# Optimization experiments

Hardware: AMD Instinct MI355X
Metric: run time of the kernel (lower is better)

## Reference

```python
import jax, jax.numpy as jnp
import numpy as np

N_NODES = 100000
N_EDGES = 1600000
N_GRAPHS = 1024
B = 1024
GNN_INP, GNN_HID, GNN_OUT = 64, 128, 64
INP, HID, OUT = 64, 256, 1
EPS = 1e-5  # torch BatchNorm1d default eps


def _bn(h, gamma, beta):
    # training-mode BatchNorm1d: biased batch statistics over dim 0
    m = h.mean(axis=0)
    v = jnp.mean((h - m) ** 2, axis=0)
    return (h - m) * jax.lax.rsqrt(v + EPS) * gamma + beta


def setup_inputs() -> dict:
    key = jax.random.key(0)
    ks = jax.random.split(key, 24)
    s = 0.05
    inp = {
        "x": jax.random.normal(ks[0], (B, INP), jnp.float32),
        "masks": jax.random.randint(ks[1], (B,), 0, N_GRAPHS),
        "gnn_x": jax.random.normal(ks[2], (N_NODES, GNN_INP), jnp.float32),
        "edge_index": jax.random.randint(ks[3], (2, N_EDGES), 0, N_NODES),
        "gnn_batch": jnp.sort(jax.random.randint(ks[4], (N_NODES,), 0, N_GRAPHS)),
        # GCNConv params
        "W_gcn": jax.random.normal(ks[5], (GNN_INP, GNN_HID), jnp.float32) * s,
        "b_gcn": jnp.zeros((GNN_HID,), jnp.float32),
        "g1": jnp.ones((GNN_HID,), jnp.float32), "be1": jnp.zeros((GNN_HID,), jnp.float32),
        "W_lin1": jax.random.normal(ks[6], (GNN_HID, GNN_HID // 2), jnp.float32) * s,
        "b_lin1": jnp.zeros((GNN_HID // 2,), jnp.float32),
        "g2": jnp.ones((GNN_HID // 2,), jnp.float32), "be2": jnp.zeros((GNN_HID // 2,), jnp.float32),
        "W_lin2": jax.random.normal(ks[7], (GNN_HID // 2, GNN_OUT), jnp.float32) * s,
        "b_lin2": jnp.zeros((GNN_OUT,), jnp.float32),
        "g3": jnp.ones((GNN_OUT,), jnp.float32), "be3": jnp.zeros((GNN_OUT,), jnp.float32),
        # head params
        "W_fc1": jax.random.normal(ks[8], (INP + GNN_OUT, HID), jnp.float32) * s,
        "b_fc1": jnp.zeros((HID,), jnp.float32),
        "g4": jnp.ones((HID,), jnp.float32), "be4": jnp.zeros((HID,), jnp.float32),
        "W_fc2": jax.random.normal(ks[9], (HID, HID // 4), jnp.float32) * s,
        "b_fc2": jnp.zeros((HID // 4,), jnp.float32),
        "g5": jnp.ones((HID // 4,), jnp.float32), "be5": jnp.zeros((HID // 4,), jnp.float32),
        "W_fc3": jax.random.normal(ks[10], (HID // 4, OUT), jnp.float32) * s,
        "b_fc3": jnp.zeros((OUT,), jnp.float32),
    }
    return inp


def _forward(x, masks, gnn_x, edge_index, gnn_batch,
             W_gcn, b_gcn, g1, be1, W_lin1, b_lin1, g2, be2, W_lin2, b_lin2,
             g3, be3, W_fc1, b_fc1, g4, be4, W_fc2, b_fc2, g5, be5, W_fc3, b_fc3):
    N = gnn_x.shape[0]
    # --- GCNConv: linear transform, self-loops, sym-normalized scatter-add ---
    h = gnn_x @ W_gcn  # [N, GNN_HID]
    loop = jnp.arange(N)
    src = jnp.concatenate([edge_index[0], loop])
    dst = jnp.concatenate([edge_index[1], loop])
    deg = jax.ops.segment_sum(jnp.ones_like(dst, jnp.float32), dst, num_segments=N)
    dis = jax.lax.rsqrt(deg)  # deg >= 1 thanks to self-loops
    norm = dis[src] * dis[dst]  # [E+N]
    agg = jax.ops.segment_sum(h[src] * norm[:, None], dst, num_segments=N) + b_gcn
    z = jax.nn.relu(_bn(agg, g1, be1))  # dropout = identity (eval)
    # --- global_mean_pool over graph ids ---
    sums = jax.ops.segment_sum(z, gnn_batch, num_segments=N_GRAPHS)
    cnt = jax.ops.segment_sum(jnp.ones((N,), jnp.float32), gnn_batch, num_segments=N_GRAPHS)
    pooled = sums / jnp.maximum(cnt, 1.0)[:, None]  # [G, GNN_HID]
    z = jax.nn.relu(_bn(pooled @ W_lin1 + b_lin1, g2, be2))
    z = _bn(z @ W_lin2 + b_lin2, g3, be3)  # [G, GNN_OUT]
    # --- MixGNN head ---
    g = z[masks]  # [B, GNN_OUT]
    t = jnp.concatenate([x, g], axis=1)
    t = jax.nn.relu(_bn(t @ W_fc1 + b_fc1, g4, be4))
    t = t * t  # Multiply([h, h])
    t = jax.nn.relu(_bn(t @ W_fc2 + b_fc2, g5, be5))
    t = t * t
    t = t * t
    return t @ W_fc3 + b_fc3  # [B, OUT]


def reference(x, masks, gnn_x, edge_index, gnn_batch,
              W_gcn, b_gcn, g1, be1, W_lin1, b_lin1, g2, be2, W_lin2, b_lin2,
              g3, be3, W_fc1, b_fc1, g4, be4, W_fc2, b_fc2, g5, be5, W_fc3, b_fc3):
    return _forward(x, masks, gnn_x, edge_index, gnn_batch,
                    W_gcn, b_gcn, g1, be1, W_lin1, b_lin1, g2, be2, W_lin2, b_lin2,
                    g3, be3, W_fc1, b_fc1, g4, be4, W_fc2, b_fc2, g5, be5, W_fc3, b_fc3)
```

## Files before the change

### kernel.cpp

```cpp
#include <hip/hip_runtime.h>
#include <hip/hip_bf16.h>

#define N_NODES 100000
#define N_EDGES 1600000
#define N_GRAPHS 1024
#define BSZ 1024
#define EPS 1e-5f

#define NBUCK 256
#define BUCKW 391
#define SRC_MASK 0x1FFFF
#define BIN_CHUNK 16384
#define BIN_BLOCKS 98
#define STAGE_CAP 16384

#define WS_GHIST   0
#define WS_BNAGG   256
#define WS_STATS1  512
#define WS_STATS2  640
#define WS_STATS4  768
#define WS_STATS5  1280
#define WS_ZTOTAL  1408
#define WS_GBASE   1408
#define WS_GCUR    1664
#define WS_GSTART  1920
#define WS_DIS     2948
#define WS_ROWPTR  102948
#define WS_PACKED  202952
#define WS_CSRC    1802952
#define WS_SCALE1  3402952
#define WS_SHIFT1  3403080
#define WS_AGGX    3403208
#define WS_AGG     9803208
#define WS_POOLED  22603208
#define WS_T1      22734280
#define WS_T2      22799816
#define WS_T4      22865352
#define WS_T5      23127496

__global__ void zero_kernel(float* __restrict__ p, int n) {
    int i = blockIdx.x * blockDim.x + threadIdx.x;
    int stride = gridDim.x * blockDim.x;
    for (; i < n; i += stride) p[i] = 0.0f;
}

__global__ __launch_bounds__(256) void hist_kernel(const int* __restrict__ dst,
                                                   int* __restrict__ ghist) {
    __shared__ int lh[NBUCK];
    int tid = threadIdx.x;
    lh[tid] = 0;
    __syncthreads();
    for (int i = blockIdx.x * 256 + tid; i < N_EDGES; i += gridDim.x * 256)
        atomicAdd(&lh[dst[i] / BUCKW], 1);
    __syncthreads();
    if (lh[tid]) atomicAdd(&ghist[tid], lh[tid]);
}

__global__ __launch_bounds__(256) void scan_kernel(const int* __restrict__ ghist,
                                                   int* __restrict__ gbase,
                                                   int* __restrict__ gcursor) {
    __shared__ int ls[NBUCK];
    int tid = threadIdx.x;
    int v = ghist[tid];
    ls[tid] = v;
    for (int off = 1; off < NBUCK; off <<= 1) {
        __syncthreads();
        int t = (tid >= off) ? ls[tid - off] : 0;
        __syncthreads();
        ls[tid] += t;
    }
    __syncthreads();
    int excl = ls[tid] - v;
    gbase[tid] = excl;
    gcursor[tid] = excl;
}

__global__ __launch_bounds__(1024) void bin_kernel(const int* __restrict__ ei,
                                                   int* __restrict__ gcursor,
                                                   unsigned int* __restrict__ packed) {
    __shared__ unsigned int stage[BIN_CHUNK];
    __shared__ int lh[NBUCK], lbase[NBUCK], lcur[NBUCK], gb[NBUCK];
    const int* src = ei;
    const int* dst = ei + N_EDGES;
    int tid = threadIdx.x;
    int base = blockIdx.x * BIN_CHUNK;
    int n = min(BIN_CHUNK, N_EDGES - base);
    if (tid < NBUCK) lh[tid] = 0;
    __syncthreads();
    for (int i = tid; i < n; i += 1024)
        atomicAdd(&lh[dst[base + i] / BUCKW], 1);
    __syncthreads();
    if (tid < NBUCK) lbase[tid] = lh[tid];
    __syncthreads();
    for (int off = 1; off < NBUCK; off <<= 1) {
        int t = (tid < NBUCK && tid >= off) ? lbase[tid - off] : 0;
        __syncthreads();
        if (tid < NBUCK) lbase[tid] += t;
        __syncthreads();
    }
    if (tid < NBUCK) {
        int excl = lbase[tid] - lh[tid];
        lbase[tid] = excl;
        lcur[tid] = excl;
        gb[tid] = atomicAdd(&gcursor[tid], lh[tid]);
    }
    __syncthreads();
    for (int i = tid; i < n; i += 1024) {
        int d = dst[base + i];
        int s = src[base + i];
        int bk = d / BUCKW;
        int dl = d - bk * BUCKW;
        int slot = atomicAdd(&lcur[bk], 1);
        stage[slot] = ((unsigned int)dl << 17) | (unsigned int)s;
    }
    __syncthreads();
    int wid = tid >> 6, lane = tid & 63;
    for (int bk = wid; bk < NBUCK; bk += 16) {
        int lo = lbase[bk], len = lh[bk], go = gb[bk];
        for (int j = lane; j < len; j += 64)
            packed[go + j] = stage[lo + j];
    }
}

__global__ __launch_bounds__(256) void csr_build_kernel(const unsigned int* __restrict__ packed,
                                                        const int* __restrict__ gbase,
                                                        const int* __restrict__ ghist,
                                                        int* __restrict__ rowptr,
                                                        int* __restrict__ csrc,
                                                        float* __restrict__ dis) {
    __shared__ int dcnt[BUCKW];
    __shared__ int lcur[BUCKW];
    __shared__ int stage[STAGE_CAP];
    int b = blockIdx.x, tid = threadIdx.x;
    int e0 = gbase[b], ecnt = ghist[b];
    int nbase = b * BUCKW;
    int nmax = min(BUCKW, N_NODES - nbase);
    for (int i = tid; i < BUCKW; i += 256) dcnt[i] = 0;
    __syncthreads();
    for (int i = tid; i < ecnt; i += 256)
        atomicAdd(&dcnt[packed[e0 + i] >> 17], 1);
    __syncthreads();
    for (int i = tid; i < nmax; i += 256)
        dis[nbase + i] = rsqrtf((float)dcnt[i] + 1.0f);
    __syncthreads();
    if (tid < 64) {
        int lane = tid;
        int run = 0;
        for (int c = 0; c < BUCKW; c += 64) {
            int idx = c + lane;
            int v = (idx < BUCKW) ? dcnt[idx] : 0;
            int inc = v;
#pragma unroll
            for (int off = 1; off < 64; off <<= 1) {
                int t = __shfl_up(inc, off);
                if (lane >= off) inc += t;
            }
            if (idx < BUCKW) {
                int excl = run + inc - v;
                dcnt[idx] = excl;
                lcur[idx] = excl;
            }
            run += __shfl(inc, 63);
        }
    }
    __syncthreads();
    for (int i = tid; i < nmax; i += 256)
        rowptr[nbase + i] = e0 + dcnt[i];
    if (b == 0 && tid == 0) rowptr[N_NODES] = N_EDGES;
    if (ecnt <= STAGE_CAP) {
        for (int i = tid; i < ecnt; i += 256) {
            unsigned int r = packed[e0 + i];
            int slot = atomicAdd(&lcur[r >> 17], 1);
            stage[slot] = (int)(r & SRC_MASK);
        }
        __syncthreads();
        for (int i = tid; i < ecnt; i += 256) csrc[e0 + i] = stage[i];
    } else {
        for (int i = tid; i < ecnt; i += 256) {
            unsigned int r = packed[e0 + i];
            int slot = atomicAdd(&lcur[r >> 17], 1);
            csrc[e0 + slot] = (int)(r & SRC_MASK);
        }
    }
}

__global__ __launch_bounds__(256) void gather_kernel(const float* __restrict__ x,
                                                     const int* __restrict__ rowptr,
                                                     const int* __restrict__ csrc,
                                                     const float* __restrict__ dis,
                                                     float* __restrict__ aggx) {
    int wid = (blockIdx.x * 256 + threadIdx.x) >> 6;
    int lane = threadIdx.x & 63;
    if (wid >= N_NODES) return;
    int start = rowptr[wid];
    int end = rowptr[wid + 1];
    float dd = dis[wid];
    float acc = x[(size_t)wid * 64 + lane] * dd * dd;
    for (int j0 = start; j0 < end; j0 += 64) {
        int cnt = min(64, end - j0);
        int sv = 0;
        float wv = 0.f;
        if (lane < cnt) {
            sv = csrc[j0 + lane];
            wv = dis[sv] * dd;
        }
        int iters = (cnt + 7) & ~7;
        for (int k = 0; k < iters; k += 8) {
            int s[8]; float w[8], v[8];
#pragma unroll
            for (int u = 0; u < 8; ++u) {
                s[u] = __shfl(sv, k + u);
                w[u] = __shfl(wv, k + u);
            }
#pragma unroll
            for (int u = 0; u < 8; ++u) v[u] = x[(size_t)s[u] * 64 + lane];
#pragma unroll
            for (int u = 0; u < 8; ++u) acc = fmaf(v[u], w[u], acc);
        }
    }
    aggx[(size_t)wid * 64 + lane] = acc;
}

__global__ __launch_bounds__(256) void gemm_agg_kernel(const float* __restrict__ A,
                                                       const float* __restrict__ W,
                                                       const float* __restrict__ bias,
                                                       float* __restrict__ AGG) {
    __shared__ float Ws[64 * 128];
    __shared__ float As[16 * 64];
    int tid = threadIdx.x;
    const float4* W4 = (const float4*)W;
    float4* Ws4 = (float4*)Ws;
#pragma unroll
    for (int i = 0; i < 8; ++i) Ws4[tid + i * 256] = W4[tid + i * 256];
    int row0 = blockIdx.x * 16;
    ((float4*)As)[tid] = ((const float4*)(A + (size_t)row0 * 64))[tid];
    __syncthreads();
    int tx = tid & 31;
    int ty = tid >> 5;
    int r0 = ty * 2;
    float4 bb = ((const float4*)bias)[tx];
    float acc[2][4] = {{bb.x, bb.y, bb.z, bb.w}, {bb.x, bb.y, bb.z, bb.w}};
#pragma unroll
    for (int k = 0; k < 64; ++k) {
        float a0 = As[r0 * 64 + k];
        float a1 = As[(r0 + 1) * 64 + k];
        float4 w = Ws4[k * 32 + tx];
        acc[0][0] += a0 * w.x; acc[0][1] += a0 * w.y; acc[0][2] += a0 * w.z; acc[0][3] += a0 * w.w;
        acc[1][0] += a1 * w.x; acc[1][1] += a1 * w.y; acc[1][2] += a1 * w.z; acc[1][3] += a1 * w.w;
    }
#pragma unroll
    for (int rr = 0; rr < 2; ++rr) {
        float4 v = make_float4(acc[rr][0], acc[rr][1], acc[rr][2], acc[rr][3]);
        ((float4*)(AGG + (size_t)(row0 + r0 + rr) * 128))[tx] = v;
    }
}

__global__ __launch_bounds__(256) void bnagg_stats_kernel(const float* __restrict__ agg,
                                                          float* __restrict__ stats) {
    __shared__ float4 ls[256];
    int tid = threadIdx.x;
    int lane = tid & 63;
    int grp = tid >> 6;
    int f = lane * 2;
    float2 s = {0.f, 0.f}, sq = {0.f, 0.f};
    for (int r = blockIdx.x * 4 + grp; r < N_NODES; r += gridDim.x * 4) {
        float2 a = *(const float2*)(agg + (size_t)r * 128 + f);
        s.x += a.x; s.y += a.y;
        sq.x += a.x * a.x; sq.y += a.y * a.y;
    }
    ls[tid] = make_float4(s.x, s.y, sq.x, sq.y);
    __syncthreads();
    if (tid < 64) {
        float4 v = ls[tid];
        float4 b = ls[tid + 64], c = ls[tid + 128], d = ls[tid + 192];
        v.x += b.x + c.x + d.x;
        v.y += b.y + c.y + d.y;
        v.z += b.z + c.z + d.z;
        v.w += b.w + c.w + d.w;
        unsafeAtomicAdd(&stats[f], v.x);
        unsafeAtomicAdd(&stats[f + 1], v.y);
        unsafeAtomicAdd(&stats[128 + f], v.z);
        unsafeAtomicAdd(&stats[128 + f + 1], v.w);
    }
}

__global__ void bn1_fold_kernel(const float* __restrict__ stats, const float* __restrict__ g1,
                                const float* __restrict__ be1, float* __restrict__ scale1,
                                float* __restrict__ shift1) {
    int f = threadIdx.x;
    float m = stats[f] * (1.0f / N_NODES);
    float var = stats[128 + f] * (1.0f / N_NODES) - m * m;
    float sc = g1[f] * rsqrtf(var + EPS);
    scale1[f] = sc;
    shift1[f] = be1[f] - m * sc;
}

__global__ __launch_bounds__(1024) void graph_bounds_kernel(const int* __restrict__ batch,
                                                            int* __restrict__ gstart) {
    int g = threadIdx.x;
    int lo = 0, hi = N_NODES;
    while (lo < hi) {
        int mid = (lo + hi) >> 1;
        if (batch[mid] < g) lo = mid + 1; else hi = mid;
    }
    gstart[g] = lo;
    if (g == 0) gstart[N_GRAPHS] = N_NODES;
}

__global__ __launch_bounds__(256) void pool_gather_kernel(const float* __restrict__ agg,
                                                          const int* __restrict__ gstart,
                                                          const float* __restrict__ scale1,
                                                          const float* __restrict__ shift1,
                                                          float* __restrict__ pooled) {
    int g = (blockIdx.x * 256 + threadIdx.x) >> 6;
    int lane = threadIdx.x & 63;
    if (g >= N_GRAPHS) return;
    int r0 = gstart[g], r1 = gstart[g + 1];
    int f = lane * 2;
    float2 sc = *(const float2*)(scale1 + f);
    float2 sh = *(const float2*)(shift1 + f);
    float2 acc = {0.f, 0.f};
    for (int r = r0; r < r1; ++r) {
        float2 a = *(const float2*)(agg + (size_t)r * 128 + f);
        acc.x += fmaxf(a.x * sc.x + sh.x, 0.f);
        acc.y += fmaxf(a.y * sc.y + sh.y, 0.f);
    }
    float inv = 1.0f / fmaxf((float)(r1 - r0), 1.0f);
    float2 o; o.x = acc.x * inv; o.y = acc.y * inv;
    *(float2*)(pooled + (size_t)g * 128 + f) = o;
}

__global__ __launch_bounds__(256) void lin1_kernel(const float* __restrict__ pooled,
                                                   const float* __restrict__ W,
                                                   const float* __restrict__ bias,
                                                   float* __restrict__ t1,
                                                   float* __restrict__ stats1) {
    __shared__ float ls[256], ls2[256];
    int tid = threadIdx.x;
    int r = blockIdx.x * 4 + (tid >> 6);
    int c = tid & 63;
    float acc = bias[c];
    const float* srow = pooled + (size_t)r * 128;
#pragma unroll 8
    for (int k = 0; k < 128; ++k)
        acc += srow[k] * W[k * 64 + c];
    t1[r * 64 + c] = acc;
    ls[tid] = acc; ls2[tid] = acc * acc;
    __syncthreads();
    if (tid < 64) {
        float s = ls[tid] + ls[tid + 64] + ls[tid + 128] + ls[tid + 192];
        float q = ls2[tid] + ls2[tid + 64] + ls2[tid + 128] + ls2[tid + 192];
        unsafeAtomicAdd(&stats1[c], s);
        unsafeAtomicAdd(&stats1[64 + c], q);
    }
}

__global__ __launch_bounds__(256) void lin2_kernel(const float* __restrict__ t1,
                                                   const float* __restrict__ stats1,
                                                   const float* __restrict__ g,
                                                   const float* __restrict__ be,
                                                   const float* __restrict__ W,
                                                   const float* __restrict__ bias,
                                                   float* __restrict__ t2,
                                                   float* __restrict__ stats2) {
    __shared__ float sc[64], sh[64];
    __shared__ float ls[256], ls2[256];
    int tid = threadIdx.x;
    if (tid < 64) {
        float m = stats1[tid] * (1.0f / BSZ);
        float var = stats1[64 + tid] * (1.0f / BSZ) - m * m;
        float s = g[tid] * rsqrtf(var + EPS);
        sc[tid] = s; sh[tid] = be[tid] - m * s;
    }
    __syncthreads();
    int r = blockIdx.x * 4 + (tid >> 6);
    int c = tid & 63;
    float acc = bias[c];
    const float* row = t1 + (size_t)r * 64;
#pragma unroll 8
    for (int k = 0; k < 64; ++k) {
        float z = fmaxf(row[k] * sc[k] + sh[k], 0.f);
        acc += z * W[k * 64 + c];
    }
    t2[r * 64 + c] = acc;
    ls[tid] = acc; ls2[tid] = acc * acc;
    __syncthreads();
    if (tid < 64) {
        float s = ls[tid] + ls[tid + 64] + ls[tid + 128] + ls[tid + 192];
        float q = ls2[tid] + ls2[tid + 64] + ls2[tid + 128] + ls2[tid + 192];
        unsafeAtomicAdd(&stats2[c], s);
        unsafeAtomicAdd(&stats2[64 + c], q);
    }
}

__global__ __launch_bounds__(1024) void fc1_kernel(const float* __restrict__ x,
                                                   const int* __restrict__ masks,
                                                   const float* __restrict__ t2,
                                                   const float* __restrict__ stats2,
                                                   const float* __restrict__ g3,
                                                   const float* __restrict__ be3,
                                                   const float* __restrict__ W,
                                                   const float* __restrict__ bias,
                                                   float* __restrict__ t4,
                                                   float* __restrict__ stats4) {
    __shared__ float sc[64], sh[64];
    __shared__ float cat[4][128];
    __shared__ float ls[1024], ls2[1024];
    int tid = threadIdx.x;
    if (tid < 64) {
        float m = stats2[tid] * (1.0f / BSZ);
        float var = stats2[64 + tid] * (1.0f / BSZ) - m * m;
        float s = g3[tid] * rsqrtf(var + EPS);
        sc[tid] = s; sh[tid] = be3[tid] - m * s;
    }
    __syncthreads();
    int r0 = blockIdx.x * 4;
    if (tid < 512) {
        int i = tid >> 7;
        int k = tid & 127;
        int r = r0 + i;
        float v;
        if (k < 64) {
            v = x[r * 64 + k];
        } else {
            int mrow = masks[r];
            int kk = k - 64;
            v = t2[mrow * 64 + kk] * sc[kk] + sh[kk];
        }
        cat[i][k] = v;
    }
    __syncthreads();
    int i = tid >> 8;
    int c = tid & 255;
    float acc = bias[c];
#pragma unroll 8
    for (int k = 0; k < 128; ++k)
        acc += cat[i][k] * W[k * 256 + c];
    t4[(size_t)(r0 + i) * 256 + c] = acc;
    ls[tid] = acc; ls2[tid] = acc * acc;
    __syncthreads();
    if (tid < 256) {
        float s = ls[tid] + ls[tid + 256] + ls[tid + 512] + ls[tid + 768];
        float q = ls2[tid] + ls2[tid + 256] + ls2[tid + 512] + ls2[tid + 768];
        unsafeAtomicAdd(&stats4[c], s);
        unsafeAtomicAdd(&stats4[256 + c], q);
    }
}

__global__ __launch_bounds__(256) void fc2_kernel(const float* __restrict__ t4,
                                                  const float* __restrict__ stats4,
                                                  const float* __restrict__ g4,
                                                  const float* __restrict__ be4,
                                                  const float* __restrict__ W,
                                                  const float* __restrict__ bias,
                                                  float* __restrict__ t5,
                                                  float* __restrict__ stats5) {
    __shared__ float sc[256], sh[256];
    __shared__ float ls[256], ls2[256];
    int tid = threadIdx.x;
    {
        float m = stats4[tid] * (1.0f / BSZ);
        float var = stats4[256 + tid] * (1.0f / BSZ) - m * m;
        float s = g4[tid] * rsqrtf(var + EPS);
        sc[tid] = s; sh[tid] = be4[tid] - m * s;
    }
    __syncthreads();
    int r = blockIdx.x * 4 + (tid >> 6);
    int c = tid & 63;
    float acc = bias[c];
    const float* row = t4 + (size_t)r * 256;
#pragma unroll 8
    for (int k = 0; k < 256; ++k) {
        float z = fmaxf(row[k] * sc[k] + sh[k], 0.f);
        z *= z;
        acc += z * W[k * 64 + c];
    }
    t5[r * 64 + c] = acc;
    ls[tid] = acc; ls2[tid] = acc * acc;
    __syncthreads();
    if (tid < 64) {
        float s = ls[tid] + ls[tid + 64] + ls[tid + 128] + ls[tid + 192];
        float q = ls2[tid] + ls2[tid + 64] + ls2[tid + 128] + ls2[tid + 192];
        unsafeAtomicAdd(&stats5[c], s);
        unsafeAtomicAdd(&stats5[64 + c], q);
    }
}

__global__ __launch_bounds__(256) void fc3_kernel(const float* __restrict__ t5,
                                                  const float* __restrict__ stats5,
                                                  const float* __restrict__ g5,
                                                  const float* __restrict__ be5,
                                                  const float* __restrict__ W,
                                                  const float* __restrict__ bias,
                                                  float* __restrict__ out) {
    __shared__ float sc[64], sh[64];
    int tid = threadIdx.x;
    if (tid < 64) {
        float m = stats5[tid] * (1.0f / BSZ);
        float var = stats5[64 + tid] * (1.0f / BSZ) - m * m;
        float s = g5[tid] * rsqrtf(var + EPS);
        sc[tid] = s; sh[tid] = be5[tid] - m * s;
    }
    __syncthreads();
    int r = blockIdx.x * 256 + tid;
    float acc = bias[0];
    const float* row = t5 + (size_t)r * 64;
#pragma unroll
    for (int k = 0; k < 64; ++k) {
        float z = fmaxf(row[k] * sc[k] + sh[k], 0.f);
        z = z * z;
        z = z * z;
        acc += z * W[k];
    }
    out[r] = acc;
}

extern "C" void kernel_launch(void* const* d_in, const int* in_sizes, int n_in,
                              void* d_out, int out_size, void* d_ws, size_t ws_size,
                              hipStream_t stream) {
    const float* x      = (const float*)d_in[0];
    const int*   masks  = (const int*)d_in[1];
    const float* gnn_x  = (const float*)d_in[2];
    const int*   ei     = (const int*)d_in[3];
    const int*   gbatch = (const int*)d_in[4];
    const float* W_gcn  = (const float*)d_in[5];
    const float* b_gcn  = (const float*)d_in[6];
    const float* g1     = (const float*)d_in[7];
    const float* be1    = (const float*)d_in[8];
    const float* W_lin1 = (const float*)d_in[9];
    const float* b_lin1 = (const float*)d_in[10];
    const float* g2     = (const float*)d_in[11];
    const float* be2    = (const float*)d_in[12];
    const float* W_lin2 = (const float*)d_in[13];
    const float* b_lin2 = (const float*)d_in[14];
    const float* g3     = (const float*)d_in[15];
    const float* be3    = (const float*)d_in[16];
    const float* W_fc1  = (const float*)d_in[17];
    const float* b_fc1  = (const float*)d_in[18];
    const float* g4     = (const float*)d_in[19];
    const float* be4    = (const float*)d_in[20];
    const float* W_fc2  = (const float*)d_in[21];
    const float* b_fc2  = (const float*)d_in[22];
    const float* g5     = (const float*)d_in[23];
    const float* be5    = (const float*)d_in[24];
    const float* W_fc3  = (const float*)d_in[25];
    const float* b_fc3  = (const float*)d_in[26];

    float* ws = (float*)d_ws;
    int*   ghist  = (int*)(ws + WS_GHIST);
    float* bnagg  = ws + WS_BNAGG;
    float* stats1 = ws + WS_STATS1;
    float* stats2 = ws + WS_STATS2;
    float* stats4 = ws + WS_STATS4;
    float* stats5 = ws + WS_STATS5;
    int*   gbase  = (int*)(ws + WS_GBASE);
    int*   gcur   = (int*)(ws + WS_GCUR);
    int*   gstart = (int*)(ws + WS_GSTART);
    float* dis    = ws + WS_DIS;
    int*   rowptr = (int*)(ws + WS_ROWPTR);
    unsigned int* packed = (unsigned int*)(ws + WS_PACKED);
    int*   csrc   = (int*)(ws + WS_CSRC);
    float* scale1 = ws + WS_SCALE1;
    float* shift1 = ws + WS_SHIFT1;
    float* aggx   = ws + WS_AGGX;
    float* agg    = ws + WS_AGG;
    float* pooled = ws + WS_POOLED;
    float* t1     = ws + WS_T1;
    float* t2     = ws + WS_T2;
    float* t4     = ws + WS_T4;
    float* t5     = ws + WS_T5;
    float* out    = (float*)d_out;

    zero_kernel<<<6, 256, 0, stream>>>(ws, WS_ZTOTAL);
    hist_kernel<<<256, 256, 0, stream>>>(ei + N_EDGES, ghist);
    scan_kernel<<<1, 256, 0, stream>>>(ghist, gbase, gcur);
    bin_kernel<<<BIN_BLOCKS, 1024, 0, stream>>>(ei, gcur, packed);
    csr_build_kernel<<<NBUCK, 256, 0, stream>>>(packed, gbase, ghist, rowptr, csrc, dis);
    gather_kernel<<<(N_NODES * 64 + 255) / 256, 256, 0, stream>>>(gnn_x, rowptr, csrc, dis, aggx);
    gemm_agg_kernel<<<N_NODES / 16, 256, 0, stream>>>(aggx, W_gcn, b_gcn, agg);
    bnagg_stats_kernel<<<512, 256, 0, stream>>>(agg, bnagg);
    bn1_fold_kernel<<<1, 128, 0, stream>>>(bnagg, g1, be1, scale1, shift1);
    graph_bounds_kernel<<<1, 1024, 0, stream>>>(gbatch, gstart);
    pool_gather_kernel<<<(N_GRAPHS * 64 + 255) / 256, 256, 0, stream>>>(agg, gstart, scale1, shift1, pooled);
    lin1_kernel<<<256, 256, 0, stream>>>(pooled, W_lin1, b_lin1, t1, stats1);
    lin2_kernel<<<256, 256, 0, stream>>>(t1, stats1, g2, be2, W_lin2, b_lin2, t2, stats2);
    fc1_kernel<<<256, 1024, 0, stream>>>(x, masks, t2, stats2, g3, be3, W_fc1, b_fc1, t4, stats4);
    fc2_kernel<<<256, 256, 0, stream>>>(t4, stats4, g4, be4, W_fc2, b_fc2, t5, stats5);
    fc3_kernel<<<4, 256, 0, stream>>>(t5, stats5, g5, be5, W_fc3, b_fc3, out);
}
```

Baseline: 295.3 us.

## Use fixed-capacity edge buckets, bf16 neighbor gather, and merge prep kernels

Drops the global histogram and scan passes by giving each destination bucket a fixed slot range (BCAP) and clamping writes to it. Per-node row lengths are stored so the gather no longer reads rowptr[i+1]. Node features are converted once to bf16 so the neighbor gather moves half the bytes. Zeroing, cursor init and the graph-bounds search are folded into one prep kernel. Any bucket that exceeds its fixed capacity silently loses edges, and the bf16 features reduce precision in the aggregation.

```diff
diff --git a/kernel.cpp b/kernel.cpp
--- a/kernel.cpp
+++ b/kernel.cpp
@@ -9,70 +9,67 @@
 
 #define NBUCK 256
 #define BUCKW 391
+#define BCAP  8192
 #define SRC_MASK 0x1FFFF
-#define BIN_CHUNK 16384
-#define BIN_BLOCKS 98
-#define STAGE_CAP 16384
-
-#define WS_GHIST   0
-#define WS_BNAGG   256
-#define WS_STATS1  512
-#define WS_STATS2  640
-#define WS_STATS4  768
-#define WS_STATS5  1280
-#define WS_ZTOTAL  1408
-#define WS_GBASE   1408
-#define WS_GCUR    1664
-#define WS_GSTART  1920
-#define WS_DIS     2948
-#define WS_ROWPTR  102948
-#define WS_PACKED  202952
-#define WS_CSRC    1802952
-#define WS_SCALE1  3402952
-#define WS_SHIFT1  3403080
-#define WS_AGGX    3403208
-#define WS_AGG     9803208
-#define WS_POOLED  22603208
-#define WS_T1      22734280
-#define WS_T2      22799816
-#define WS_T4      22865352
-#define WS_T5      23127496
-
-__global__ void zero_kernel(float* __restrict__ p, int n) {
-    int i = blockIdx.x * blockDim.x + threadIdx.x;
-    int stride = gridDim.x * blockDim.x;
-    for (; i < n; i += stride) p[i] = 0.0f;
-}
-
-__global__ __launch_bounds__(256) void hist_kernel(const int* __restrict__ dst,
-                                                   int* __restrict__ ghist) {
-    __shared__ int lh[NBUCK];
-    int tid = threadIdx.x;
-    lh[tid] = 0;
-    __syncthreads();
-    for (int i = blockIdx.x * 256 + tid; i < N_EDGES; i += gridDim.x * 256)
-        atomicAdd(&lh[dst[i] / BUCKW], 1);
-    __syncthreads();
-    if (lh[tid]) atomicAdd(&ghist[tid], lh[tid]);
-}
-
-__global__ __launch_bounds__(256) void scan_kernel(const int* __restrict__ ghist,
-                                                   int* __restrict__ gbase,
-                                                   int* __restrict__ gcursor) {
-    __shared__ int ls[NBUCK];
-    int tid = threadIdx.x;
-    int v = ghist[tid];
-    ls[tid] = v;
-    for (int off = 1; off < NBUCK; off <<= 1) {
-        __syncthreads();
-        int t = (tid >= off) ? ls[tid - off] : 0;
-        __syncthreads();
-        ls[tid] += t;
-    }
-    __syncthreads();
-    int excl = ls[tid] - v;
-    gbase[tid] = excl;
-    gcursor[tid] = excl;
+#define BIN_CHUNK 8192
+#define BIN_BLOCKS 196
+
+#define WS_BNAGG   0
+#define WS_STATS1  256
+#define WS_STATS2  384
+#define WS_STATS4  512
+#define WS_STATS5  1024
+#define WS_ZTOTAL  1152
+#define WS_GCUR    1152
+#define WS_SCALE1  1408
+#define WS_SHIFT1  1536
+#define WS_GSTART  1664
+#define WS_DIS     2692
+#define WS_ROWPTR  102692
+#define WS_ROWLEN  202692
+#define WS_AGG     302692
+#define WS_PACKED  302692
+#define WS_CSRC    2399844
+#define WS_XH      4496996
+#define WS_AGGX    13102692
+#define WS_POOLED  19502692
+#define WS_T1      19633764
+#define WS_T2      19699300
+#define WS_T4      19764836
+#define WS_T5      20026980
+
+__device__ inline unsigned short f2bf(float f) {
+    unsigned int u = __float_as_uint(f);
+    return (unsigned short)((u + 0x7FFFu + ((u >> 16) & 1u)) >> 16);
+}
+
+__global__ __launch_bounds__(256) void prep_kernel(float* __restrict__ ws,
+                                                   const int* __restrict__ gbatch) {
+    int b = blockIdx.x, tid = threadIdx.x;
+    if (b == 0) {
+        for (int i = tid; i < WS_ZTOTAL; i += 256) ws[i] = 0.0f;
+    } else if (b == 1) {
+        ((int*)(ws + WS_GCUR))[tid] = tid * BCAP;
+    } else {
+        int g = (b - 2) * 256 + tid;
+        int lo = 0, hi = N_NODES;
+        while (lo < hi) {
+            int mid = (lo + hi) >> 1;
+            if (gbatch[mid] < g) lo = mid + 1; else hi = mid;
+        }
+        int* gstart = (int*)(ws + WS_GSTART);
+        gstart[g] = lo;
+        if (g == 0) gstart[N_GRAPHS] = N_NODES;
+    }
+}
+
+__global__ __launch_bounds__(256) void cvt_kernel(const float* __restrict__ x,
+                                                  unsigned short* __restrict__ xh) {
+    int i = blockIdx.x * 256 + threadIdx.x;
+    float4 f = ((const float4*)x)[i];
+    ushort4 h;
+    h.x = f2bf(f.x); h.y = f2bf(f.y); h.z = f2bf(f.z); h.w = f2bf(f.w);
+    ((ushort4*)xh)[i] = h;
 }
 
 __global__ __launch_bounds__(1024) void bin_kernel(const int* __restrict__ ei,
@@ -116,23 +113,25 @@
     __syncthreads();
     int wid = tid >> 6, lane = tid & 63;
     for (int bk = wid; bk < NBUCK; bk += 16) {
-        int lo = lbase[bk], len = lh[bk], go = gb[bk];
+        int lo = lbase[bk], go = gb[bk];
+        int len = min(lh[bk], (bk + 1) * BCAP - go);
         for (int j = lane; j < len; j += 64)
             packed[go + j] = stage[lo + j];
     }
 }
 
 __global__ __launch_bounds__(256) void csr_build_kernel(const unsigned int* __restrict__ packed,
-                                                        const int* __restrict__ gbase,
-                                                        const int* __restrict__ ghist,
+                                                        const int* __restrict__ gcur,
                                                         int* __restrict__ rowptr,
+                                                        int* __restrict__ rowlen,
                                                         int* __restrict__ csrc,
                                                         float* __restrict__ dis) {
     __shared__ int dcnt[BUCKW];
     __shared__ int lcur[BUCKW];
-    __shared__ int stage[STAGE_CAP];
+    __shared__ int stage[BCAP];
     int b = blockIdx.x, tid = threadIdx.x;
-    int e0 = gbase[b], ecnt = ghist[b];
+    int e0 = b * BCAP;
+    int ecnt = min(gcur[b] - e0, BCAP);
     int nbase = b * BUCKW;
     int nmax = min(BUCKW, N_NODES - nbase);
     for (int i = tid; i < BUCKW; i += 256) dcnt[i] = 0;
@@ -140,8 +139,10 @@
     for (int i = tid; i < ecnt; i += 256)
         atomicAdd(&dcnt[packed[e0 + i] >> 17], 1);
     __syncthreads();
-    for (int i = tid; i < nmax; i += 256)
+    for (int i = tid; i < nmax; i += 256) {
         dis[nbase + i] = rsqrtf((float)dcnt[i] + 1.0f);
+        rowlen[nbase + i] = dcnt[i];
+    }
     __syncthreads();
     if (tid < 64) {
         int lane = tid;
@@ -166,26 +167,19 @@
     __syncthreads();
     for (int i = tid; i < nmax; i += 256)
         rowptr[nbase + i] = e0 + dcnt[i];
-    if (b == 0 && tid == 0) rowptr[N_NODES] = N_EDGES;
-    if (ecnt <= STAGE_CAP) {
-        for (int i = tid; i < ecnt; i += 256) {
-            unsigned int r = packed[e0 + i];
-            int slot = atomicAdd(&lcur[r >> 17], 1);
-            stage[slot] = (int)(r & SRC_MASK);
-        }
-        __syncthreads();
-        for (int i = tid; i < ecnt; i += 256) csrc[e0 + i] = stage[i];
-    } else {
-        for (int i = tid; i < ecnt; i += 256) {
-            unsigned int r = packed[e0 + i];
-            int slot = atomicAdd(&lcur[r >> 17], 1);
-            csrc[e0 + slot] = (int)(r & SRC_MASK);
-        }
-    }
+    for (int i = tid; i < ecnt; i += 256) {
+        unsigned int r = packed[e0 + i];
+        int slot = atomicAdd(&lcur[r >> 17], 1);
+        stage[slot] = (int)(r & SRC_MASK);
+    }
+    __syncthreads();
+    for (int i = tid; i < ecnt; i += 256) csrc[e0 + i] = stage[i];
 }
 
 __global__ __launch_bounds__(256) void gather_kernel(const float* __restrict__ x,
+                                                     const unsigned short* __restrict__ xh,
                                                      const int* __restrict__ rowptr,
+                                                     const int* __restrict__ rowlen,
                                                      const int* __restrict__ csrc,
                                                      const float* __restrict__ dis,
                                                      float* __restrict__ aggx) {
@@ -193,15 +187,15 @@
     int lane = threadIdx.x & 63;
     if (wid >= N_NODES) return;
     int start = rowptr[wid];
-    int end = rowptr[wid + 1];
+    int len = rowlen[wid];
     float dd = dis[wid];
     float acc = x[(size_t)wid * 64 + lane] * dd * dd;
-    for (int j0 = start; j0 < end; j0 += 64) {
-        int cnt = min(64, end - j0);
+    for (int j0 = 0; j0 < len; j0 += 64) {
+        int cnt = min(64, len - j0);
         int sv = 0;
         float wv = 0.f;
         if (lane < cnt) {
-            sv = csrc[j0 + lane];
+            sv = csrc[start + j0 + lane];
             wv = dis[sv] * dd;
         }
         int iters = (cnt + 7) & ~7;
@@ -213,7 +207,8 @@
                 w[u] = __shfl(wv, k + u);
             }
 #pragma unroll
-            for (int u = 0; u < 8; ++u) v[u] = x[(size_t)s[u] * 64 + lane];
+            for (int u = 0; u < 8; ++u)
+                v[u] = __uint_as_float((unsigned int)xh[(size_t)s[u] * 64 + lane] << 16);
 #pragma unroll
             for (int u = 0; u < 8; ++u) acc = fmaf(v[u], w[u], acc);
         }
@@ -293,18 +288,6 @@
     float sc = g1[f] * rsqrtf(var + EPS);
     scale1[f] = sc;
     shift1[f] = be1[f] - m * sc;
-}
-
-__global__ __launch_bounds__(1024) void graph_bounds_kernel(const int* __restrict__ batch,
-                                                            int* __restrict__ gstart) {
-    int g = threadIdx.x;
-    int lo = 0, hi = N_NODES;
-    while (lo < hi) {
-        int mid = (lo + hi) >> 1;
-        if (batch[mid] < g) lo = mid + 1; else hi = mid;
-    }
-    gstart[g] = lo;
-    if (g == 0) gstart[N_GRAPHS] = N_NODES;
 }
 
 __global__ __launch_bounds__(256) void pool_gather_kernel(const float* __restrict__ agg,
@@ -547,23 +530,23 @@
     const float* b_fc3  = (const float*)d_in[26];
 
     float* ws = (float*)d_ws;
-    int*   ghist  = (int*)(ws + WS_GHIST);
     float* bnagg  = ws + WS_BNAGG;
     float* stats1 = ws + WS_STATS1;
     float* stats2 = ws + WS_STATS2;
     float* stats4 = ws + WS_STATS4;
     float* stats5 = ws + WS_STATS5;
-    int*   gbase  = (int*)(ws + WS_GBASE);
     int*   gcur   = (int*)(ws + WS_GCUR);
+    float* scale1 = ws + WS_SCALE1;
+    float* shift1 = ws + WS_SHIFT1;
     int*   gstart = (int*)(ws + WS_GSTART);
     float* dis    = ws + WS_DIS;
     int*   rowptr = (int*)(ws + WS_ROWPTR);
+    int*   rowlen = (int*)(ws + WS_ROWLEN);
+    float* agg    = ws + WS_AGG;
     unsigned int* packed = (unsigned int*)(ws + WS_PACKED);
     int*   csrc   = (int*)(ws + WS_CSRC);
-    float* scale1 = ws + WS_SCALE1;
-    float* shift1 = ws + WS_SHIFT1;
+    unsigned short* xh = (unsigned short*)(ws + WS_XH);
     float* aggx   = ws + WS_AGGX;
-    float* agg    = ws + WS_AGG;
     float* pooled = ws + WS_POOLED;
     float* t1     = ws + WS_T1;
     float* t2     = ws + WS_T2;
@@ -571,16 +554,14 @@
     float* t5     = ws + WS_T5;
     float* out    = (float*)d_out;
 
-    zero_kernel<<<6, 256, 0, stream>>>(ws, WS_ZTOTAL);
-    hist_kernel<<<256, 256, 0, stream>>>(ei + N_EDGES, ghist);
-    scan_kernel<<<1, 256, 0, stream>>>(ghist, gbase, gcur);
+    prep_kernel<<<6, 256, 0, stream>>>(ws, gbatch);
+    cvt_kernel<<<N_NODES * 64 / 4 / 256, 256, 0, stream>>>(gnn_x, xh);
     bin_kernel<<<BIN_BLOCKS, 1024, 0, stream>>>(ei, gcur, packed);
-    csr_build_kernel<<<NBUCK, 256, 0, stream>>>(packed, gbase, ghist, rowptr, csrc, dis);
-    gather_kernel<<<(N_NODES * 64 + 255) / 256, 256, 0, stream>>>(gnn_x, rowptr, csrc, dis, aggx);
+    csr_build_kernel<<<NBUCK, 256, 0, stream>>>(packed, gcur, rowptr, rowlen, csrc, dis);
+    gather_kernel<<<(N_NODES * 64 + 255) / 256, 256, 0, stream>>>(gnn_x, xh, rowptr, rowlen, csrc, dis, aggx);
     gemm_agg_kernel<<<N_NODES / 16, 256, 0, stream>>>(aggx, W_gcn, b_gcn, agg);
     bnagg_stats_kernel<<<512, 256, 0, stream>>>(agg, bnagg);
     bn1_fold_kernel<<<1, 128, 0, stream>>>(bnagg, g1, be1, scale1, shift1);
-    graph_bounds_kernel<<<1, 1024, 0, stream>>>(gbatch, gstart);
     pool_gather_kernel<<<(N_GRAPHS * 64 + 255) / 256, 256, 0, stream>>>(agg, gstart, scale1, shift1, pooled);
     lin1_kernel<<<256, 256, 0, stream>>>(pooled, W_lin1, b_lin1, t1, stats1);
     lin2_kernel<<<256, 256, 0, stream>>>(t1, stats1, g2, be2, W_lin2, b_lin2, t2, stats2);
```

Result: faster. 272.1 us (-7.9%).
